# Kernel tuning notes

Measured on AMD Instinct MI355X. Metric: run time of the kernel, lower is better.

## Reference

```python
import jax, jax.numpy as jnp
import numpy as np

N = 50000
E = 800000
IN_C = 128
HEADS = 2
HID = 64  # out_channels // heads (concat=True)
NEG_SLOPE = 0.2


def setup_inputs() -> dict:
    key = jax.random.key(0)
    ks = jax.random.split(key, 8)
    x = jax.random.normal(ks[0], (N, IN_C), dtype=jnp.float32)
    edge_index = jax.random.randint(ks[1], (2, E), 0, N, dtype=jnp.int64)
    edge_weight = jax.random.uniform(ks[2], (E,), dtype=jnp.float32)
    s = 1.0 / np.sqrt(IN_C)
    W_l = jax.random.normal(ks[3], (IN_C, HEADS * HID), dtype=jnp.float32) * s
    b_l = jnp.zeros((HEADS * HID,), dtype=jnp.float32)
    W_r = jax.random.normal(ks[4], (IN_C, HEADS * HID), dtype=jnp.float32) * s
    b_r = jnp.zeros((HEADS * HID,), dtype=jnp.float32)
    att = jax.random.normal(ks[5], (HEADS, HID), dtype=jnp.float32) * (1.0 / np.sqrt(HID))
    bias = jnp.zeros((HEADS * HID,), dtype=jnp.float32)
    return {"x": x, "edge_index": edge_index, "edge_weight": edge_weight,
            "W_l": W_l, "b_l": b_l, "W_r": W_r, "b_r": b_r,
            "att": att, "bias": bias}


def reference(x, edge_index, edge_weight, W_l, b_l, W_r, b_r, att, bias):
    src = edge_index[0]  # source nodes j (messages flow j -> i)
    dst = edge_index[1]  # destination nodes i
    # per-head linear transforms: [N, H, C]
    x_l = (x @ W_l + b_l).reshape(N, HEADS, HID)
    x_r = (x @ W_r + b_r).reshape(N, HEADS, HID)
    # GATv2 edge score: att . LeakyReLU(x_l[j] + x_r[i])  -> [E, H]
    e = x_l[src] + x_r[dst]
    e = jnp.where(e >= 0, e, NEG_SLOPE * e)
    alpha = jnp.einsum('ehc,hc->eh', e, att)
    # segment softmax over incoming edges of each destination node
    amax = jax.ops.segment_max(alpha, dst, num_segments=N)  # [N, H]
    alpha = jnp.exp(alpha - amax[dst])
    denom = jax.ops.segment_sum(alpha, dst, num_segments=N)  # [N, H]
    alpha = alpha / (denom[dst] + 1e-16)
    # scatter-add aggregation of weighted source features
    out = jax.ops.segment_sum(x_l[src] * alpha[:, :, None], dst, num_segments=N)
    out = out.reshape(N, HEADS * HID) + bias
    return jnp.tanh(out)
```

## Files before the change

### kernel.cpp

```cpp
#include <hip/hip_runtime.h>
#include <hip/hip_fp16.h>
#include <math.h>

#define N_NODES 50000
#define E_EDGES 800000
#define IN_CH   128
#define OUT_CH  128
#define HID     64
#define NEG_SLOPE 0.2f
#define NBLK_SCAN ((N_NODES + 255) / 256)
#define XS_STRIDE 136

typedef _Float16 half8 __attribute__((ext_vector_type(8)));
typedef _Float16 h2 __attribute__((ext_vector_type(2)));
typedef float f32x2 __attribute__((ext_vector_type(2)));
typedef float f32x4 __attribute__((ext_vector_type(4)));

template<int CTRL>
__device__ __forceinline__ float dpp_add(float a) {
    int t = __builtin_amdgcn_update_dpp(0, __float_as_int(a), CTRL, 0xF, 0xF, true);
    return a + __int_as_float(t);
}
#define REDUCE16(a)                                                          \
    a = dpp_add<0x128>(a); a = dpp_add<0x124>(a);                            \
    a = dpp_add<0x122>(a); a = dpp_add<0x121>(a);

__global__ __launch_bounds__(256) void convW_kernel(
    const float* __restrict__ Wl, const float* __restrict__ bl,
    const float* __restrict__ Wr, const float* __restrict__ br,
    __half* __restrict__ wfrag, float* __restrict__ bcat,
    int* __restrict__ counts, int* __restrict__ done) {
    const int gid = blockIdx.x * 256 + threadIdx.x;
    if (gid < N_NODES) counts[gid] = 0;
    if (gid == 0) *done = 0;
    if (gid >= 4096) return;
    const int n = gid & 255;
    const int c = gid >> 8;
    const int t = n >> 4, q16 = n & 15, s = c >> 2, kg = c & 3;
    const int k0 = c * 8;
    const float* __restrict__ Wsrc = (n < 128) ? Wl : Wr;
    const int col = n & 127;
    half8 h;
    #pragma unroll
    for (int j = 0; j < 8; ++j) h[j] = (_Float16)Wsrc[(k0 + j) * 128 + col];
    ((half8*)wfrag)[((t * 4 + s) * 4 + kg) * 16 + q16] = h;
    if (c == 0) bcat[n] = (n < 128) ? bl[col] : br[col];
}

__global__ void count_kernel(const int* __restrict__ ei, int* __restrict__ counts,
                             int* __restrict__ rank) {
    int t = blockIdx.x * blockDim.x + threadIdx.x;
    if (t * 2 < E_EDGES) {
        int2 d = *(const int2*)(ei + E_EDGES + t * 2);
        int2 r;
        r.x = atomicAdd(&counts[d.x], 1);
        r.y = atomicAdd(&counts[d.y], 1);
        *(int2*)(rank + t * 2) = r;
    }
}

__global__ __launch_bounds__(256) void linear_mfma_kernel(
    const float* __restrict__ x, const __half* __restrict__ wfrag,
    const float* __restrict__ bcat,
    __half* __restrict__ xl16, float* __restrict__ xr) {
    __shared__ __align__(16) __half xs[64 * XS_STRIDE];
    const int tid  = threadIdx.x;
    const int lane = tid & 63;
    const int wv   = tid >> 6;
    const int nodeBase = blockIdx.x * 64;

    {
        const float4* __restrict__ x4 = (const float4*)(x + (size_t)nodeBase * IN_CH);
        #pragma unroll
        for (int i = 0; i < 8; ++i) {
            const int idx = tid + i * 256;
            const int row = idx >> 5;
            const int c   = (idx & 31) * 4;
            float4 v = {0.0f, 0.0f, 0.0f, 0.0f};
            if (nodeBase + row < N_NODES) v = x4[idx];
            __half2 h01 = __floats2half2_rn(v.x, v.y);
            __half2 h23 = __floats2half2_rn(v.z, v.w);
            uint2 pk;
            pk.x = *(unsigned int*)&h01;
            pk.y = *(unsigned int*)&h23;
            *(uint2*)&xs[row * XS_STRIDE + c] = pk;
        }
    }
    __syncthreads();

    const int q16 = lane & 15;
    const int kg  = lane >> 4;

    const half8* __restrict__ wf8 = (const half8*)wfrag;
    half8 b[4][4];
    #pragma unroll
    for (int t = 0; t < 4; ++t)
        #pragma unroll
        for (int s = 0; s < 4; ++s)
            b[t][s] = wf8[(((wv * 4 + t) * 4 + s) * 4 + kg) * 16 + q16];

    #pragma unroll
    for (int m = 0; m < 4; ++m) {
        f32x4 acc[4];
        #pragma unroll
        for (int t = 0; t < 4; ++t) acc[t] = (f32x4){0.0f, 0.0f, 0.0f, 0.0f};
        #pragma unroll
        for (int s = 0; s < 4; ++s) {
            const half8 a = *(const half8*)&xs[(m * 16 + q16) * XS_STRIDE + s * 32 + kg * 8];
            #pragma unroll
            for (int t = 0; t < 4; ++t)
                acc[t] = __builtin_amdgcn_mfma_f32_16x16x32_f16(a, b[t][s], acc[t], 0, 0, 0);
        }
        const int nodeRow0 = nodeBase + m * 16 + kg * 4;
        #pragma unroll
        for (int t = 0; t < 4; ++t) {
            const int col = wv * 64 + t * 16 + q16;
            const float bv = bcat[col];
            #pragma unroll
            for (int r = 0; r < 4; ++r) {
                const int node = nodeRow0 + r;
                if (node < N_NODES) {
                    const float v = acc[t][r] + bv;
                    if (col < 128) xl16[(size_t)node * 128 + col] = __float2half_rn(v);
                    else           xr[(size_t)node * 128 + (col - 128)] = v;
                }
            }
        }
    }
}

__global__ __launch_bounds__(256) void scan1_kernel(const int* __restrict__ counts,
                                                    int* __restrict__ off,
                                                    int* __restrict__ tops,
                                                    int* __restrict__ done) {
    __shared__ int s[256];
    __shared__ int ticket;
    int i = blockIdx.x * 256 + threadIdx.x;
    int v = (i < N_NODES) ? counts[i] : 0;
    s[threadIdx.x] = v;
    __syncthreads();
    for (int dlt = 1; dlt < 256; dlt <<= 1) {
        int t = (threadIdx.x >= dlt) ? s[threadIdx.x - dlt] : 0;
        __syncthreads();
        s[threadIdx.x] += t;
        __syncthreads();
    }
    if (i < N_NODES) off[i] = s[threadIdx.x] - v;
    if (threadIdx.x == 255) {
        atomicExch(&tops[blockIdx.x], s[255]);
        ticket = atomicAdd(done, 1);
    }
    __syncthreads();
    if (ticket == NBLK_SCAN - 1) {
        int tv = (threadIdx.x < NBLK_SCAN) ? atomicAdd(&tops[threadIdx.x], 0) : 0;
        s[threadIdx.x] = tv;
        __syncthreads();
        for (int dlt = 1; dlt < 256; dlt <<= 1) {
            int t = (threadIdx.x >= dlt) ? s[threadIdx.x - dlt] : 0;
            __syncthreads();
            s[threadIdx.x] += t;
            __syncthreads();
        }
        if (threadIdx.x < NBLK_SCAN) atomicExch(&tops[threadIdx.x], s[threadIdx.x] - tv);
    }
}

__global__ void scatter_kernel(const int* __restrict__ ei, const int* __restrict__ off,
                               const int* __restrict__ tops, const int* __restrict__ rank,
                               int* __restrict__ ssrc) {
    int t = blockIdx.x * blockDim.x + threadIdx.x;
    if (t * 4 >= E_EDGES) return;
    int4 d = *(const int4*)(ei + E_EDGES + t * 4);
    int4 s = *(const int4*)(ei + t * 4);
    int4 r = *(const int4*)(rank + t * 4);
    ssrc[tops[d.x >> 8] + off[d.x] + r.x] = s.x;
    ssrc[tops[d.y >> 8] + off[d.y] + r.y] = s.y;
    ssrc[tops[d.z >> 8] + off[d.z] + r.z] = s.z;
    ssrc[tops[d.w >> 8] + off[d.w] + r.w] = s.w;
}

__global__ __launch_bounds__(256) void node_agg_kernel(
    const __half* __restrict__ xl16, const float* __restrict__ xr,
    const float* __restrict__ att,
    const int* __restrict__ off, const int* __restrict__ counts,
    const int* __restrict__ tops, const int* __restrict__ ssrc,
    const float* __restrict__ bias, float* __restrict__ out) {
    const int node = (blockIdx.x * blockDim.x + threadIdx.x) >> 6;
    const int lane = threadIdx.x & 63;
    if (node >= N_NODES) return;
    const int half = lane >> 5;
    const int cl   = lane & 31;

    const uint2* __restrict__ xlh = (const uint2*)xl16;
    const float4 xrv  = ((const float4*)xr)[node * 32 + cl];
    const float4 attv = ((const float4*)att)[cl];
    const h2 xr01  = {(_Float16)xrv.x, (_Float16)xrv.y};
    const h2 xr23  = {(_Float16)xrv.z, (_Float16)xrv.w};
    const h2 att01 = {(_Float16)attv.x, (_Float16)attv.y};
    const h2 att23 = {(_Float16)attv.z, (_Float16)attv.w};
    const h2 ns2   = {(_Float16)NEG_SLOPE, (_Float16)NEG_SLOPE};

    const int cnt = counts[node];
    const int o   = tops[node >> 8] + off[node];

    float d = 0.0f;
    float4 acc = {0.0f, 0.0f, 0.0f, 0.0f};

#define SCOREH(raw, aout)                                                    \
    {                                                                        \
        h2 v01 = *(h2*)&raw.x;                                               \
        h2 v23 = *(h2*)&raw.y;                                               \
        h2 s01 = v01 + xr01;                                                 \
        h2 s23 = v23 + xr23;                                                 \
        h2 l01 = __builtin_elementwise_max(s01, s01 * ns2);                  \
        h2 l23 = __builtin_elementwise_max(s23, s23 * ns2);                  \
        aout = __builtin_amdgcn_fdot2(l01, att01,                            \
               __builtin_amdgcn_fdot2(l23, att23, 0.0f, false), false);      \
    }
#define ACCUM(raw, wgt)                                                      \
    {                                                                        \
        f32x2 f01 = __builtin_convertvector(*(h2*)&raw.x, f32x2);            \
        f32x2 f23 = __builtin_convertvector(*(h2*)&raw.y, f32x2);            \
        d += wgt;                                                            \
        acc.x = fmaf(wgt, f01.x, acc.x);                                     \
        acc.y = fmaf(wgt, f01.y, acc.y);                                     \
        acc.z = fmaf(wgt, f23.x, acc.z);                                     \
        acc.w = fmaf(wgt, f23.y, acc.w);                                     \
    }

    int k = 0;
    for (; k + 4 <= cnt; k += 4) {
        const int sA = ssrc[o + k + half];
        const int sB = ssrc[o + k + 2 + half];
        const uint2 rA = xlh[sA * 32 + cl];
        const uint2 rB = xlh[sB * 32 + cl];
        float a0, a1;
        SCOREH(rA, a0);
        SCOREH(rB, a1);
        REDUCE16(a0);
        REDUCE16(a1);
        const float eA = __expf(a0);
        const float eB = __expf(a1);
        ACCUM(rA, eA);
        ACCUM(rB, eB);
    }
    for (; k < cnt; k += 2) {
        const int eidx = k + half;
        const bool valid = (eidx < cnt);
        const int src = ssrc[o + (valid ? eidx : 0)];
        const uint2 raw = xlh[src * 32 + cl];
        float a;
        SCOREH(raw, a);
        REDUCE16(a);
        const float ev = valid ? __expf(a) : 0.0f;
        ACCUM(raw, ev);
    }
#undef SCOREH
#undef ACCUM
    acc.x += __shfl_xor(acc.x, 32);
    acc.y += __shfl_xor(acc.y, 32);
    acc.z += __shfl_xor(acc.z, 32);
    acc.w += __shfl_xor(acc.w, 32);
    d     += __shfl_xor(d, 32);

    if (lane < 32) {
        const float4 bv = ((const float4*)bias)[cl];
        const float inv = 1.0f / (d + 1e-16f);
        float4 r;
        float t;
        t = __expf(2.0f * fmaf(acc.x, inv, bv.x)); r.x = (t - 1.0f) / (t + 1.0f);
        t = __expf(2.0f * fmaf(acc.y, inv, bv.y)); r.y = (t - 1.0f) / (t + 1.0f);
        t = __expf(2.0f * fmaf(acc.z, inv, bv.z)); r.z = (t - 1.0f) / (t + 1.0f);
        t = __expf(2.0f * fmaf(acc.w, inv, bv.w)); r.w = (t - 1.0f) / (t + 1.0f);
        ((float4*)out)[node * 32 + cl] = r;
    }
}

extern "C" void kernel_launch(void* const* d_in, const int* in_sizes, int n_in,
                              void* d_out, int out_size, void* d_ws, size_t ws_size,
                              hipStream_t stream) {
    const float* x    = (const float*)d_in[0];
    const int*   ei   = (const int*)d_in[1];
    const float* Wl   = (const float*)d_in[3];
    const float* bl   = (const float*)d_in[4];
    const float* Wr   = (const float*)d_in[5];
    const float* br   = (const float*)d_in[6];
    const float* att  = (const float*)d_in[7];
    const float* bias = (const float*)d_in[8];
    float* out = (float*)d_out;

    char* ws = (char*)d_ws;
    __half* xl16  = (__half*)ws;  ws += (size_t)N_NODES * OUT_CH * 2;
    float*  xr    = (float*)ws;   ws += (size_t)N_NODES * OUT_CH * 4;
    __half* wfrag = (__half*)ws;  ws += (size_t)256 * 128 * 2;
    float*  bcat  = (float*)ws;   ws += 256 * 4;
    int*   counts = (int*)ws;     ws += (size_t)N_NODES * 4;
    int*   off    = (int*)ws;     ws += (size_t)N_NODES * 4;
    int*   tops   = (int*)ws;     ws += 256 * 4;
    int*   done   = (int*)ws;     ws += 16;
    int*   rank   = (int*)ws;     ws += (size_t)E_EDGES * 4;
    int*   ssrc   = (int*)ws;     ws += (size_t)E_EDGES * 4;

    const int pairBlocks = (E_EDGES / 2 + 255) / 256;

    convW_kernel<<<NBLK_SCAN, 256, 0, stream>>>(Wl, bl, Wr, br, wfrag, bcat, counts, done);
    linear_mfma_kernel<<<(N_NODES + 63) / 64, 256, 0, stream>>>(x, wfrag, bcat, xl16, xr);
    count_kernel<<<pairBlocks, 256, 0, stream>>>(ei, counts, rank);
    scan1_kernel<<<NBLK_SCAN, 256, 0, stream>>>(counts, off, tops, done);
    scatter_kernel<<<(E_EDGES / 4 + 255) / 256, 256, 0, stream>>>(ei, off, tops, rank, ssrc);
    node_agg_kernel<<<(N_NODES + 3) / 4, 256, 0, stream>>>(
        xl16, xr, att, off, counts, tops, ssrc, bias, out);
}
```

Baseline: 126.0 us.

## Store x_r in fp16 and process four edges per wave with 16-byte gathers

```diff
diff --git a/kernel.cpp b/kernel.cpp
--- a/kernel.cpp
+++ b/kernel.cpp
@@ -21,9 +21,8 @@
     int t = __builtin_amdgcn_update_dpp(0, __float_as_int(a), CTRL, 0xF, 0xF, true);
     return a + __int_as_float(t);
 }
-#define REDUCE16(a)                                                          \
-    a = dpp_add<0x128>(a); a = dpp_add<0x124>(a);                            \
-    a = dpp_add<0x122>(a); a = dpp_add<0x121>(a);
+#define REDUCE8(a)                                                           \
+    a = dpp_add<0xB1>(a); a = dpp_add<0x4E>(a); a = dpp_add<0x141>(a);
 
 __global__ __launch_bounds__(256) void convW_kernel(
     const float* __restrict__ Wl, const float* __restrict__ bl,
@@ -62,7 +61,7 @@
 __global__ __launch_bounds__(256) void linear_mfma_kernel(
     const float* __restrict__ x, const __half* __restrict__ wfrag,
     const float* __restrict__ bcat,
-    __half* __restrict__ xl16, float* __restrict__ xr) {
+    __half* __restrict__ xl16, __half* __restrict__ xr16) {
     __shared__ __align__(16) __half xs[64 * XS_STRIDE];
     const int tid  = threadIdx.x;
     const int lane = tid & 63;
@@ -116,14 +115,13 @@
         for (int t = 0; t < 4; ++t) {
             const int col = wv * 64 + t * 16 + q16;
             const float bv = bcat[col];
+            __half* __restrict__ dstp = (col < 128) ? xl16 : xr16;
+            const int dcol = col & 127;
             #pragma unroll
             for (int r = 0; r < 4; ++r) {
                 const int node = nodeRow0 + r;
-                if (node < N_NODES) {
-                    const float v = acc[t][r] + bv;
-                    if (col < 128) xl16[(size_t)node * 128 + col] = __float2half_rn(v);
-                    else           xr[(size_t)node * 128 + (col - 128)] = v;
-                }
+                if (node < N_NODES)
+                    dstp[(size_t)node * 128 + dcol] = __float2half_rn(acc[t][r] + bv);
             }
         }
     }
@@ -180,7 +178,7 @@
 }
 
 __global__ __launch_bounds__(256) void node_agg_kernel(
-    const __half* __restrict__ xl16, const float* __restrict__ xr,
+    const __half* __restrict__ xl16, const __half* __restrict__ xr16,
     const float* __restrict__ att,
     const int* __restrict__ off, const int* __restrict__ counts,
     const int* __restrict__ tops, const int* __restrict__ ssrc,
@@ -188,91 +186,105 @@
     const int node = (blockIdx.x * blockDim.x + threadIdx.x) >> 6;
     const int lane = threadIdx.x & 63;
     if (node >= N_NODES) return;
-    const int half = lane >> 5;
-    const int cl   = lane & 31;
-
-    const uint2* __restrict__ xlh = (const uint2*)xl16;
-    const float4 xrv  = ((const float4*)xr)[node * 32 + cl];
-    const float4 attv = ((const float4*)att)[cl];
-    const h2 xr01  = {(_Float16)xrv.x, (_Float16)xrv.y};
-    const h2 xr23  = {(_Float16)xrv.z, (_Float16)xrv.w};
-    const h2 att01 = {(_Float16)attv.x, (_Float16)attv.y};
-    const h2 att23 = {(_Float16)attv.z, (_Float16)attv.w};
-    const h2 ns2   = {(_Float16)NEG_SLOPE, (_Float16)NEG_SLOPE};
+    const int qw = lane >> 4;
+    const int ql = lane & 15;
+
+    const uint4* __restrict__ xlh = (const uint4*)xl16;
+    const uint4 xq = ((const uint4*)xr16)[node * 16 + ql];
+    const h2 xq0 = *(h2*)&xq.x, xq1 = *(h2*)&xq.y, xq2 = *(h2*)&xq.z, xq3 = *(h2*)&xq.w;
+    const float4 atA = ((const float4*)att)[ql * 2];
+    const float4 atB = ((const float4*)att)[ql * 2 + 1];
+    const h2 at0 = {(_Float16)atA.x, (_Float16)atA.y};
+    const h2 at1 = {(_Float16)atA.z, (_Float16)atA.w};
+    const h2 at2 = {(_Float16)atB.x, (_Float16)atB.y};
+    const h2 at3 = {(_Float16)atB.z, (_Float16)atB.w};
+    const h2 ns2 = {(_Float16)NEG_SLOPE, (_Float16)NEG_SLOPE};
 
     const int cnt = counts[node];
     const int o   = tops[node >> 8] + off[node];
 
     float d = 0.0f;
-    float4 acc = {0.0f, 0.0f, 0.0f, 0.0f};
-
-#define SCOREH(raw, aout)                                                    \
+    float av[8] = {0.0f, 0.0f, 0.0f, 0.0f, 0.0f, 0.0f, 0.0f, 0.0f};
+
+#define SCOREH(rq, aout)                                                     \
     {                                                                        \
-        h2 v01 = *(h2*)&raw.x;                                               \
-        h2 v23 = *(h2*)&raw.y;                                               \
-        h2 s01 = v01 + xr01;                                                 \
-        h2 s23 = v23 + xr23;                                                 \
-        h2 l01 = __builtin_elementwise_max(s01, s01 * ns2);                  \
-        h2 l23 = __builtin_elementwise_max(s23, s23 * ns2);                  \
-        aout = __builtin_amdgcn_fdot2(l01, att01,                            \
-               __builtin_amdgcn_fdot2(l23, att23, 0.0f, false), false);      \
-    }
-#define ACCUM(raw, wgt)                                                      \
+        h2 v0 = *(h2*)&rq.x, v1 = *(h2*)&rq.y, v2 = *(h2*)&rq.z, v3 = *(h2*)&rq.w; \
+        h2 s0 = v0 + xq0, s1 = v1 + xq1, s2 = v2 + xq2, s3 = v3 + xq3;       \
+        h2 l0 = __builtin_elementwise_max(s0, s0 * ns2);                     \
+        h2 l1 = __builtin_elementwise_max(s1, s1 * ns2);                     \
+        h2 l2 = __builtin_elementwise_max(s2, s2 * ns2);                     \
+        h2 l3 = __builtin_elementwise_max(s3, s3 * ns2);                     \
+        aout = __builtin_amdgcn_fdot2(l0, at0,                               \
+               __builtin_amdgcn_fdot2(l1, at1,                               \
+               __builtin_amdgcn_fdot2(l2, at2,                               \
+               __builtin_amdgcn_fdot2(l3, at3, 0.0f, false), false), false), false); \
+    }
+#define ACCUM(rq, wgt)                                                       \
     {                                                                        \
-        f32x2 f01 = __builtin_convertvector(*(h2*)&raw.x, f32x2);            \
-        f32x2 f23 = __builtin_convertvector(*(h2*)&raw.y, f32x2);            \
+        f32x2 f0 = __builtin_convertvector(*(h2*)&rq.x, f32x2);              \
+        f32x2 f1 = __builtin_convertvector(*(h2*)&rq.y, f32x2);              \
+        f32x2 f2 = __builtin_convertvector(*(h2*)&rq.z, f32x2);              \
+        f32x2 f3 = __builtin_convertvector(*(h2*)&rq.w, f32x2);              \
         d += wgt;                                                            \
-        acc.x = fmaf(wgt, f01.x, acc.x);                                     \
-        acc.y = fmaf(wgt, f01.y, acc.y);                                     \
-        acc.z = fmaf(wgt, f23.x, acc.z);                                     \
-        acc.w = fmaf(wgt, f23.y, acc.w);                                     \
+        av[0] = fmaf(wgt, f0.x, av[0]); av[1] = fmaf(wgt, f0.y, av[1]);      \
+        av[2] = fmaf(wgt, f1.x, av[2]); av[3] = fmaf(wgt, f1.y, av[3]);      \
+        av[4] = fmaf(wgt, f2.x, av[4]); av[5] = fmaf(wgt, f2.y, av[5]);      \
+        av[6] = fmaf(wgt, f3.x, av[6]); av[7] = fmaf(wgt, f3.y, av[7]);      \
     }
 
     int k = 0;
-    for (; k + 4 <= cnt; k += 4) {
-        const int sA = ssrc[o + k + half];
-        const int sB = ssrc[o + k + 2 + half];
-        const uint2 rA = xlh[sA * 32 + cl];
-        const uint2 rB = xlh[sB * 32 + cl];
+    for (; k + 8 <= cnt; k += 8) {
+        const int iA = ssrc[o + k + qw];
+        const int iB = ssrc[o + k + 4 + qw];
+        const uint4 rA = xlh[iA * 16 + ql];
+        const uint4 rB = xlh[iB * 16 + ql];
         float a0, a1;
         SCOREH(rA, a0);
         SCOREH(rB, a1);
-        REDUCE16(a0);
-        REDUCE16(a1);
+        REDUCE8(a0);
+        REDUCE8(a1);
         const float eA = __expf(a0);
         const float eB = __expf(a1);
         ACCUM(rA, eA);
         ACCUM(rB, eB);
     }
-    for (; k < cnt; k += 2) {
-        const int eidx = k + half;
-        const bool valid = (eidx < cnt);
-        const int src = ssrc[o + (valid ? eidx : 0)];
-        const uint2 raw = xlh[src * 32 + cl];
+    for (; k < cnt; k += 4) {
+        const int e = k + qw;
+        const bool valid = (e < cnt);
+        const int idx = ssrc[o + (valid ? e : 0)];
+        const uint4 rq = xlh[idx * 16 + ql];
         float a;
-        SCOREH(raw, a);
-        REDUCE16(a);
+        SCOREH(rq, a);
+        REDUCE8(a);
         const float ev = valid ? __expf(a) : 0.0f;
-        ACCUM(raw, ev);
+        ACCUM(rq, ev);
     }
 #undef SCOREH
 #undef ACCUM
-    acc.x += __shfl_xor(acc.x, 32);
-    acc.y += __shfl_xor(acc.y, 32);
-    acc.z += __shfl_xor(acc.z, 32);
-    acc.w += __shfl_xor(acc.w, 32);
-    d     += __shfl_xor(d, 32);
-
-    if (lane < 32) {
-        const float4 bv = ((const float4*)bias)[cl];
+    #pragma unroll
+    for (int j = 0; j < 8; ++j) {
+        av[j] += __shfl_xor(av[j], 16);
+        av[j] += __shfl_xor(av[j], 32);
+    }
+    d += __shfl_xor(d, 16);
+    d += __shfl_xor(d, 32);
+
+    if (qw == 0) {
+        const float4 b0 = ((const float4*)bias)[ql * 2];
+        const float4 b1 = ((const float4*)bias)[ql * 2 + 1];
         const float inv = 1.0f / (d + 1e-16f);
-        float4 r;
+        float4 r0, r1;
         float t;
-        t = __expf(2.0f * fmaf(acc.x, inv, bv.x)); r.x = (t - 1.0f) / (t + 1.0f);
-        t = __expf(2.0f * fmaf(acc.y, inv, bv.y)); r.y = (t - 1.0f) / (t + 1.0f);
-        t = __expf(2.0f * fmaf(acc.z, inv, bv.z)); r.z = (t - 1.0f) / (t + 1.0f);
-        t = __expf(2.0f * fmaf(acc.w, inv, bv.w)); r.w = (t - 1.0f) / (t + 1.0f);
-        ((float4*)out)[node * 32 + cl] = r;
+        t = __expf(2.0f * fmaf(av[0], inv, b0.x)); r0.x = (t - 1.0f) / (t + 1.0f);
+        t = __expf(2.0f * fmaf(av[1], inv, b0.y)); r0.y = (t - 1.0f) / (t + 1.0f);
+        t = __expf(2.0f * fmaf(av[2], inv, b0.z)); r0.z = (t - 1.0f) / (t + 1.0f);
+        t = __expf(2.0f * fmaf(av[3], inv, b0.w)); r0.w = (t - 1.0f) / (t + 1.0f);
+        t = __expf(2.0f * fmaf(av[4], inv, b1.x)); r1.x = (t - 1.0f) / (t + 1.0f);
+        t = __expf(2.0f * fmaf(av[5], inv, b1.y)); r1.y = (t - 1.0f) / (t + 1.0f);
+        t = __expf(2.0f * fmaf(av[6], inv, b1.z)); r1.z = (t - 1.0f) / (t + 1.0f);
+        t = __expf(2.0f * fmaf(av[7], inv, b1.w)); r1.w = (t - 1.0f) / (t + 1.0f);
+        *(float4*)(out + (size_t)node * 128 + ql * 8)     = r0;
+        *(float4*)(out + (size_t)node * 128 + ql * 8 + 4) = r1;
     }
 }
 
@@ -291,7 +303,7 @@
 
     char* ws = (char*)d_ws;
     __half* xl16  = (__half*)ws;  ws += (size_t)N_NODES * OUT_CH * 2;
-    float*  xr    = (float*)ws;   ws += (size_t)N_NODES * OUT_CH * 4;
+    __half* xr16  = (__half*)ws;  ws += (size_t)N_NODES * OUT_CH * 2;
     __half* wfrag = (__half*)ws;  ws += (size_t)256 * 128 * 2;
     float*  bcat  = (float*)ws;   ws += 256 * 4;
     int*   counts = (int*)ws;     ws += (size_t)N_NODES * 4;
@@ -304,10 +316,10 @@
     const int pairBlocks = (E_EDGES / 2 + 255) / 256;
 
     convW_kernel<<<NBLK_SCAN, 256, 0, stream>>>(Wl, bl, Wr, br, wfrag, bcat, counts, done);
-    linear_mfma_kernel<<<(N_NODES + 63) / 64, 256, 0, stream>>>(x, wfrag, bcat, xl16, xr);
+    linear_mfma_kernel<<<(N_NODES + 63) / 64, 256, 0, stream>>>(x, wfrag, bcat, xl16, xr16);
     count_kernel<<<pairBlocks, 256, 0, stream>>>(ei, counts, rank);
     scan1_kernel<<<NBLK_SCAN, 256, 0, stream>>>(counts, off, tops, done);
     scatter_kernel<<<(E_EDGES / 4 + 255) / 256, 256, 0, stream>>>(ei, off, tops, rank, ssrc);
     node_agg_kernel<<<(N_NODES + 3) / 4, 256, 0, stream>>>(
-        xl16, xr, att, off, counts, tops, ssrc, bias, out);
-}
+        xl16, xr16, att, off, counts, tops, ssrc, bias, out);
+}
```

New measurement: 121.8 us. 1.03x faster.
